# Kernel optimization log

Hardware: AMD Instinct MI355X
Metric: run time of the kernel (lower is better)

Reference implementation:

```python
import jax, jax.numpy as jnp
import numpy as np

D, H, W = 64, 128, 128
NUM_LABELS = 2
NUM_ITERS = 5
SIGMA_SPATIAL_BLUR = 1.0   # sigma for the pure spatial Gaussian filter
BLUR_RADIUS = 2            # 5-tap separable kernel
SIGMA_BILAT_SPATIAL = 1.5  # spatial sigma of bilateral filter
SIGMA_BILAT_RANGE = 0.5    # intensity (range) sigma of bilateral filter
LOG_SQRT_2PI = 0.5 * float(np.log(2.0 * np.pi))


def _shift(x, axis, off):
    # zero-padded shift: out[i] = x[i - off] along `axis` (static off)
    if off == 0:
        return x
    pad = [(0, 0)] * x.ndim
    sl = [slice(None)] * x.ndim
    if off > 0:
        pad[axis] = (off, 0)
        sl[axis] = slice(0, x.shape[axis])
    else:
        pad[axis] = (0, -off)
        sl[axis] = slice(-off, x.shape[axis] - off)
    return jnp.pad(x, pad)[tuple(sl)]


def _shift3(x, dz, dy, dx):
    return _shift(_shift(_shift(x, 2, dz), 3, dy), 4, dx)


_offs = np.arange(-BLUR_RADIUS, BLUR_RADIUS + 1)
_k1d = np.exp(-_offs.astype(np.float64) ** 2 / (2.0 * SIGMA_SPATIAL_BLUR ** 2))
_k1d = (_k1d / _k1d.sum()).astype(np.float32)


def _gaussian_blur3d(x):
    # separable normalized Gaussian over the 3 spatial axes (zero padding)
    for ax in (2, 3, 4):
        x = sum(float(_k1d[i]) * _shift(x, ax, int(_offs[i])) for i in range(len(_offs)))
    return x


def _bilateral_weights(image):
    # precompute 27 neighbor weight maps (image is constant across CRF iterations)
    ws, offsets = [], []
    for dz in (-1, 0, 1):
        for dy in (-1, 0, 1):
            for dx in (-1, 0, 1):
                d2 = float(dz * dz + dy * dy + dx * dx)
                img_s = _shift3(image, dz, dy, dx)
                w = jnp.exp(-d2 / (2.0 * SIGMA_BILAT_SPATIAL ** 2)
                            - (image - img_s) ** 2 / (2.0 * SIGMA_BILAT_RANGE ** 2))
                ws.append(w)
                offsets.append((dz, dy, dx))
    den = sum(ws)  # (1,1,D,H,W), broadcasts over labels
    return ws, den, offsets


def _bilateral_apply(q, ws, den, offsets):
    num = sum(w * _shift3(q, dz, dy, dx) for w, (dz, dy, dx) in zip(ws, offsets))
    return num / den


def _crfrnn(image, logits, unary, spatial_w, bilateral_w, compat):
    ws, den, offsets = _bilateral_weights(image)
    cur = logits
    for _ in range(NUM_ITERS):
        qs = jax.nn.softmax(cur, axis=1)                      # (1,L,D,H,W)
        sp = _gaussian_blur3d(qs)                             # spatial message
        bl = _bilateral_apply(qs, ws, den, offsets)           # bilateral message
        msg = (jnp.einsum('lm,bmdhw->bldhw', spatial_w, sp)
               + jnp.einsum('lm,bmdhw->bldhw', bilateral_w, bl))
        pairwise = jnp.einsum('lm,bmdhw->bldhw', compat, msg)
        cur = unary - pairwise
    return jax.nn.softmax(cur, axis=1)


def setup_inputs() -> dict:
    key = jax.random.key(0)
    k1, k2, k3, k4, k5, k6 = jax.random.split(key, 6)
    image = jax.random.normal(k1, (1, 1, D, H, W), dtype=jnp.float32)
    q = jax.random.uniform(k2, (1, 1, D, H, W), dtype=jnp.float32)
    h = jnp.concatenate([1.0 - q, q], axis=1)                 # (1,2,D,H,W)
    f_1 = jax.random.normal(k3, (1, 1, D, H, W), dtype=jnp.float32)
    w_0 = jnp.zeros((1,), dtype=jnp.float32)
    spatial_ker_weights = jax.random.normal(k4, (NUM_LABELS, NUM_LABELS), dtype=jnp.float32)
    bilateral_ker_weights = jax.random.normal(k5, (NUM_LABELS, NUM_LABELS), dtype=jnp.float32)
    compatibility_matrix = jax.random.normal(k6, (NUM_LABELS, NUM_LABELS), dtype=jnp.float32)
    return {'image': image, 'h': h, 'f_1': f_1, 'w_0': w_0,
            'spatial_ker_weights': spatial_ker_weights,
            'bilateral_ker_weights': bilateral_ker_weights,
            'compatibility_matrix': compatibility_matrix}


def reference(image, h, f_1, w_0, spatial_ker_weights, bilateral_ker_weights, compatibility_matrix):
    logits = h
    log_prob = -0.5 * image * image - LOG_SQRT_2PI           # N(0,1).log_prob(image)
    unary = h * (-(w_0[0] + log_prob - f_1))                 # broadcasts (1,1,..) -> (1,2,..)
    h_new = _crfrnn(image, logits, unary, spatial_ker_weights,
                    bilateral_ker_weights, compatibility_matrix)
    return (h_new, f_1)
```

## Files before the change

kernel.cpp:

```cpp
#include <hip/hip_runtime.h>


#define DD 64
#define HH 128
#define WW 128
#define NN (DD*HH*WW)
#define PAD 264
#define TILE_WU 6912

__device__ __forceinline__ float bfac(int p, int dim) {
    const float K[5] = {0.05448868f, 0.24420134f, 0.40261995f, 0.24420134f, 0.05448868f};
    float s = 0.f;
#pragma unroll
    for (int o = -2; o <= 2; ++o) {
        int pp = p + o;
        s += (pp >= 0 && pp < dim) ? K[o + 2] : 0.f;
    }
    return s;
}

__device__ __forceinline__ void ldrow(const float* p, float* r) {
    float4 a = *(const float4*)p;
    float4 b = *(const float4*)(p + 4);
    r[0] = a.x; r[1] = a.y; r[2] = a.z; r[3] = a.w;
    r[4] = b.x; r[5] = b.y; r[6] = b.z; r[7] = b.w;
}

__global__ __launch_bounds__(256) void crf_pre(
    const float* __restrict__ img, const float* __restrict__ h,
    const float* __restrict__ f1, const float* __restrict__ w0,
    const float* __restrict__ sw, const float* __restrict__ bw,
    const float* __restrict__ cm,
    float* __restrict__ qA, float* __restrict__ P,
    float* __restrict__ M, unsigned int* __restrict__ W)
{
    const float Sc[4] = {1.f, 0.80073740f, 0.64118039f, 0.51341712f};
    __shared__ float ims[10][10][20];

    const int tid = threadIdx.x;
    const int x0 = blockIdx.x * 16, y0 = blockIdx.y * 8, z0 = blockIdx.z * 8;
    const int T = ((int)blockIdx.z * 16 + (int)blockIdx.y) * 8 + (int)blockIdx.x;

    float* imf = &ims[0][0][0];
    for (int idx = tid; idx < 2000; idx += 256) {
        int lz2 = idx / 200, r = idx - lz2 * 200, ly2 = r / 20, lx2 = r - ly2 * 20;
        int gz = z0 + lz2 - 1, gy = y0 + ly2 - 1, gx = x0 + lx2 - 1;
        float v = 0.f;
        if ((unsigned)gz < 64u && (unsigned)gy < 128u && (unsigned)gx < 128u)
            v = img[(gz << 14) + (gy << 7) + gx];
        imf[idx] = v;
    }
    __syncthreads();

    const int lx = (tid & 3) * 4;
    const int ly = (tid >> 2) & 7;
    const int lz = tid >> 5;
    const int x = x0 + lx, y = y0 + ly, z = z0 + lz;
    const int g = (z << 14) + (y << 7) + x;

    const float cd0 = cm[2] - cm[0], cd1 = cm[3] - cm[1];
    const float Ksp = cd0 * sw[0] + cd1 * sw[2];
    const float Kbl = cd0 * bw[0] + cd1 * bw[2];
    const float Bc  = cd0 * (bw[1] - bw[0]) + cd1 * (bw[3] - bw[2]);

    float rowC[8];
    ldrow(&ims[lz + 1][ly + 1][lx], rowC);
    const float Ic[4] = {rowC[1], rowC[2], rowC[3], rowC[4]};

    float den[4] = {0.f, 0.f, 0.f, 0.f}, numi[4] = {0.f, 0.f, 0.f, 0.f};
    unsigned int* __restrict__ Wt = W + T * TILE_WU;

    float rI[8];
#pragma unroll
    for (int r9 = 0; r9 < 9; ++r9) {
        const int dz = r9 / 3 - 1, dy = r9 % 3 - 1;
        ldrow(&ims[lz + 1 + dz][ly + 1 + dy][lx], rI);
        const bool zyin = ((unsigned)(z + dz) < 64u) && ((unsigned)(y + dy) < 128u);
#pragma unroll
        for (int c = 0; c < 3; ++c) {
            const int dx = c - 1;
            const float s = Sc[dz * dz + dy * dy + dx * dx];
            unsigned pack = 0;
#pragma unroll
            for (int xi = 0; xi < 4; ++xi) {
                float dd = Ic[xi] - rI[xi + c];
                float w = s * __expf(-2.f * dd * dd);
                den[xi] += w;
                bool inb = zyin && ((unsigned)(x + xi + dx) < 128u);
                numi[xi] += inb ? w : 0.f;
                pack |= ((unsigned)(w * 255.f + 0.5f)) << (8 * xi);
            }
            Wt[(r9 * 3 + c) * 256 + tid] = pack;
        }
    }

    float4 h0v = *(const float4*)&h[g];
    float4 h1v = *(const float4*)&h[NN + g];
    float4 f1v = *(const float4*)&f1[g];
    const float w00 = w0[0];
    const float bz = bfac(z, 64), by = bfac(y, 128);
    float hh0[4] = {h0v.x, h0v.y, h0v.z, h0v.w};
    float hh1[4] = {h1v.x, h1v.y, h1v.z, h1v.w};
    float ff[4]  = {f1v.x, f1v.y, f1v.z, f1v.w};
    float qv[4], Pv[4], Mv[4];
#pragma unroll
    for (int xi = 0; xi < 4; ++xi) {
        float dq = hh1[xi] - hh0[xi];
        float logp = -0.5f * Ic[xi] * Ic[xi] - 0.91893853320467274f;
        float t = -(w00 + logp - ff[xi]);
        float bones = bz * by * bfac(x + xi, 128);
        qv[xi] = 1.f / (1.f + __expf(-dq));
        Pv[xi] = dq * t - Ksp * bones - Kbl * (numi[xi] / den[xi]);
        Mv[xi] = Bc / (den[xi] * 255.f);
    }
    *(float4*)&qA[g] = {qv[0], qv[1], qv[2], qv[3]};
    *(float4*)&P[g]  = {Pv[0], Pv[1], Pv[2], Pv[3]};
    *(float4*)&M[g]  = {Mv[0], Mv[1], Mv[2], Mv[3]};
}

template <bool LAST>
__global__ __launch_bounds__(256) void crf_iter(
    const float* __restrict__ qsrc, float* __restrict__ qdst,
    const float* __restrict__ P, const float* __restrict__ M,
    const unsigned int* __restrict__ W,
    const float* __restrict__ sw, const float* __restrict__ cm,
    const float* __restrict__ f1, float* __restrict__ out)
{
    const float K0 = 0.05448868f, K1 = 0.24420134f, K2 = 0.40261995f;

    __shared__ float qs[12][12][20];
    __shared__ float t1[12][12][16];
    __shared__ float t2[12][8][16];

    const int tid = threadIdx.x;
    const int x0 = blockIdx.x * 16, y0 = blockIdx.y * 8, zB = blockIdx.z * 8;
    const int T = ((int)blockIdx.z * 16 + (int)blockIdx.y) * 8 + (int)blockIdx.x;

    const float cd0 = cm[2] - cm[0], cd1 = cm[3] - cm[1];
    const float Ac = cd0 * (sw[1] - sw[0]) + cd1 * (sw[3] - sw[2]);

    float* qf = &qs[0][0][0];
    for (int idx = tid; idx < 2880; idx += 256) {
        int lz2 = idx / 240, r = idx - lz2 * 240, ly2 = r / 20, lx2 = r - ly2 * 20;
        int gz = zB + lz2 - 2, gy = y0 + ly2 - 2, gx = x0 + lx2 - 2;
        float v = 0.f;
        if ((unsigned)gz < 64u && (unsigned)gy < 128u && (unsigned)gx < 128u)
            v = qsrc[(gz << 14) + (gy << 7) + gx];
        qf[idx] = v;
    }
    __syncthreads();

    for (int idx = tid; idx < 576; idx += 256) {
        int lz2 = idx / 48, r = idx - lz2 * 48, ly2 = r / 4, c4 = (r - ly2 * 4) * 4;
        const float* row = &qs[lz2][ly2][c4];
        float4 a = *(const float4*)row;
        float4 b = *(const float4*)(row + 4);
        float4 o;
        o.x = K0 * (a.x + b.x) + K1 * (a.y + a.w) + K2 * a.z;
        o.y = K0 * (a.y + b.y) + K1 * (a.z + b.x) + K2 * a.w;
        o.z = K0 * (a.z + b.z) + K1 * (a.w + b.y) + K2 * b.x;
        o.w = K0 * (a.w + b.w) + K1 * (b.x + b.z) + K2 * b.y;
        *(float4*)&t1[lz2][ly2][c4] = o;
    }
    __syncthreads();

    for (int idx = tid; idx < 384; idx += 256) {
        int lz2 = idx / 32, r = idx - lz2 * 32, ly2 = r / 4, c4 = (r - ly2 * 4) * 4;
        float4 r0 = *(const float4*)&t1[lz2][ly2][c4];
        float4 r1 = *(const float4*)&t1[lz2][ly2 + 1][c4];
        float4 r2 = *(const float4*)&t1[lz2][ly2 + 2][c4];
        float4 r3 = *(const float4*)&t1[lz2][ly2 + 3][c4];
        float4 r4 = *(const float4*)&t1[lz2][ly2 + 4][c4];
        float4 o;
        o.x = K0 * (r0.x + r4.x) + K1 * (r1.x + r3.x) + K2 * r2.x;
        o.y = K0 * (r0.y + r4.y) + K1 * (r1.y + r3.y) + K2 * r2.y;
        o.z = K0 * (r0.z + r4.z) + K1 * (r1.z + r3.z) + K2 * r2.z;
        o.w = K0 * (r0.w + r4.w) + K1 * (r1.w + r3.w) + K2 * r2.w;
        *(float4*)&t2[lz2][ly2][c4] = o;
    }
    __syncthreads();

    const int lx = (tid & 3) * 4;
    const int ly = (tid >> 2) & 7;
    const int lz = tid >> 5;

    float4 za = *(const float4*)&t2[lz][ly][lx];
    float4 zb = *(const float4*)&t2[lz + 1][ly][lx];
    float4 zc = *(const float4*)&t2[lz + 2][ly][lx];
    float4 zd = *(const float4*)&t2[lz + 3][ly][lx];
    float4 ze = *(const float4*)&t2[lz + 4][ly][lx];
    float sp[4];
    sp[0] = K0 * (za.x + ze.x) + K1 * (zb.x + zd.x) + K2 * zc.x;
    sp[1] = K0 * (za.y + ze.y) + K1 * (zb.y + zd.y) + K2 * zc.y;
    sp[2] = K0 * (za.z + ze.z) + K1 * (zb.z + zd.z) + K2 * zc.z;
    sp[3] = K0 * (za.w + ze.w) + K1 * (zb.w + zd.w) + K2 * zc.w;

    const int g = ((zB + lz) << 14) + ((y0 + ly) << 7) + (x0 + lx);

    const unsigned int* __restrict__ Wt = W + T * TILE_WU;
    float num[4] = {0.f, 0.f, 0.f, 0.f};
    float qrow[8];
#pragma unroll
    for (int r9 = 0; r9 < 9; ++r9) {
        const int dz = r9 / 3 - 1, dy = r9 % 3 - 1;
        ldrow(&qs[lz + 2 + dz][ly + 2 + dy][lx], qrow);
#pragma unroll
        for (int c = 0; c < 3; ++c) {
            unsigned wv = Wt[(r9 * 3 + c) * 256 + tid];
#pragma unroll
            for (int xi = 0; xi < 4; ++xi)
                num[xi] += (float)((wv >> (8 * xi)) & 0xffu) * qrow[xi + 1 + c];
        }
    }

    float4 Pv = *(const float4*)&P[g];
    float4 Mv = *(const float4*)&M[g];
    float pr[4] = {Pv.x, Pv.y, Pv.z, Pv.w};
    float mv[4] = {Mv.x, Mv.y, Mv.z, Mv.w};
    float qn[4];
#pragma unroll
    for (int xi = 0; xi < 4; ++xi) {
        float dn = pr[xi] - Ac * sp[xi] - mv[xi] * num[xi];
        qn[xi] = 1.f / (1.f + __expf(-dn));
    }

    if (!LAST) {
        float4 o = {qn[0], qn[1], qn[2], qn[3]};
        *(float4*)&qdst[g] = o;
    } else {
        float4 o1 = {qn[0], qn[1], qn[2], qn[3]};
        float4 o0 = {1.f - qn[0], 1.f - qn[1], 1.f - qn[2], 1.f - qn[3]};
        *(float4*)&out[g] = o0;
        *(float4*)&out[NN + g] = o1;
        float4 fv = *(const float4*)&f1[g];
        *(float4*)&out[2 * NN + g] = fv;
    }
}

extern "C" void kernel_launch(void* const* d_in, const int* in_sizes, int n_in,
                              void* d_out, int out_size, void* d_ws, size_t ws_size,
                              hipStream_t stream)
{
    const float* img = (const float*)d_in[0];
    const float* h   = (const float*)d_in[1];
    const float* f1  = (const float*)d_in[2];
    const float* w0  = (const float*)d_in[3];
    const float* sw  = (const float*)d_in[4];
    const float* bw  = (const float*)d_in[5];
    const float* cm  = (const float*)d_in[6];
    float* out = (float*)d_out;

    float* qA = (float*)d_ws;
    float* qB = qA + (NN + PAD);
    float* P  = qB + (NN + PAD);
    float* M  = P + (NN + PAD);
    unsigned int* W = (unsigned int*)(M + (NN + PAD));

    dim3 grid(WW / 16, HH / 8, DD / 8);
    crf_pre<<<grid, 256, 0, stream>>>(img, h, f1, w0, sw, bw, cm, qA, P, M, W);

    crf_iter<false><<<grid, 256, 0, stream>>>(qA, qB, P, M, W, sw, cm, nullptr, nullptr);
    crf_iter<false><<<grid, 256, 0, stream>>>(qB, qA, P, M, W, sw, cm, nullptr, nullptr);
    crf_iter<false><<<grid, 256, 0, stream>>>(qA, qB, P, M, W, sw, cm, nullptr, nullptr);
    crf_iter<false><<<grid, 256, 0, stream>>>(qB, qA, P, M, W, sw, cm, nullptr, nullptr);
    crf_iter<true ><<<grid, 256, 0, stream>>>(qA, nullptr, P, M, W, sw, cm, f1, out);
}
```

Baseline: 161.5 us.

## Store q in zero-padded layout for branchless vectorized halo loads and prefetch weights

Measured after the change: 175.0 us. 1.08x slower.

```diff
diff --git a/kernel.cpp b/kernel.cpp
--- a/kernel.cpp
+++ b/kernel.cpp
@@ -7,6 +7,10 @@
 #define NN (DD*HH*WW)
 #define PAD 264
 #define TILE_WU 6912
+#define XP 136
+#define SLICE (132*136)
+#define QTOT (68*SLICE)
+#define QOFF (2*SLICE + 2*XP + 4)
 
 __device__ __forceinline__ float bfac(int p, int dim) {
     const float K[5] = {0.05448868f, 0.24420134f, 0.40261995f, 0.24420134f, 0.05448868f};
@@ -26,13 +30,14 @@
     r[4] = b.x; r[5] = b.y; r[6] = b.z; r[7] = b.w;
 }
 
-__global__ __launch_bounds__(256) void crf_pre(
+__global__ __launch_bounds__(256, 4) void crf_pre(
     const float* __restrict__ img, const float* __restrict__ h,
     const float* __restrict__ f1, const float* __restrict__ w0,
     const float* __restrict__ sw, const float* __restrict__ bw,
     const float* __restrict__ cm,
-    float* __restrict__ qA, float* __restrict__ P,
-    float* __restrict__ M, unsigned int* __restrict__ W)
+    float* __restrict__ qA, float* __restrict__ qB,
+    float* __restrict__ P, float* __restrict__ M,
+    unsigned int* __restrict__ W, float* __restrict__ out)
 {
     const float Sc[4] = {1.f, 0.80073740f, 0.64118039f, 0.51341712f};
     __shared__ float ims[10][10][20];
@@ -40,6 +45,17 @@
     const int tid = threadIdx.x;
     const int x0 = blockIdx.x * 16, y0 = blockIdx.y * 8, z0 = blockIdx.z * 8;
     const int T = ((int)blockIdx.z * 16 + (int)blockIdx.y) * 8 + (int)blockIdx.x;
+
+    {
+        int gtid = T * 256 + tid;
+        for (int lin = gtid; lin < QTOT; lin += 262144) {
+            int zq = lin / SLICE, r = lin - zq * SLICE;
+            int yq = r / XP, xq = r - yq * XP;
+            bool inter = (zq >= 2 && zq < 66 && yq >= 2 && yq < 130 &&
+                          xq >= 4 && xq < 132);
+            if (!inter) { qA[lin] = 0.f; qB[lin] = 0.f; }
+        }
+    }
 
     float* imf = &ims[0][0][0];
     for (int idx = tid; idx < 2000; idx += 256) {
@@ -52,9 +68,7 @@
     }
     __syncthreads();
 
-    const int lx = (tid & 3) * 4;
-    const int ly = (tid >> 2) & 7;
-    const int lz = tid >> 5;
+    const int lx = (tid & 3) * 4, ly = (tid >> 2) & 7, lz = tid >> 5;
     const int x = x0 + lx, y = y0 + ly, z = z0 + lz;
     const int g = (z << 14) + (y << 7) + x;
 
@@ -66,10 +80,8 @@
     float rowC[8];
     ldrow(&ims[lz + 1][ly + 1][lx], rowC);
     const float Ic[4] = {rowC[1], rowC[2], rowC[3], rowC[4]};
-
     float den[4] = {0.f, 0.f, 0.f, 0.f}, numi[4] = {0.f, 0.f, 0.f, 0.f};
     unsigned int* __restrict__ Wt = W + T * TILE_WU;
-
     float rI[8];
 #pragma unroll
     for (int r9 = 0; r9 < 9; ++r9) {
@@ -97,11 +109,11 @@
     float4 h0v = *(const float4*)&h[g];
     float4 h1v = *(const float4*)&h[NN + g];
     float4 f1v = *(const float4*)&f1[g];
-    const float w00 = w0[0];
-    const float bz = bfac(z, 64), by = bfac(y, 128);
     float hh0[4] = {h0v.x, h0v.y, h0v.z, h0v.w};
     float hh1[4] = {h1v.x, h1v.y, h1v.z, h1v.w};
     float ff[4]  = {f1v.x, f1v.y, f1v.z, f1v.w};
+    const float w00 = w0[0];
+    const float bz = bfac(z, 64), by = bfac(y, 128);
     float qv[4], Pv[4], Mv[4];
 #pragma unroll
     for (int xi = 0; xi < 4; ++xi) {
@@ -113,53 +125,68 @@
         Pv[xi] = dq * t - Ksp * bones - Kbl * (numi[xi] / den[xi]);
         Mv[xi] = Bc / (den[xi] * 255.f);
     }
-    *(float4*)&qA[g] = {qv[0], qv[1], qv[2], qv[3]};
-    *(float4*)&P[g]  = {Pv[0], Pv[1], Pv[2], Pv[3]};
-    *(float4*)&M[g]  = {Mv[0], Mv[1], Mv[2], Mv[3]};
+    *(float4*)&qA[z * SLICE + y * XP + x + QOFF] = {qv[0], qv[1], qv[2], qv[3]};
+    *(float4*)&P[g] = {Pv[0], Pv[1], Pv[2], Pv[3]};
+    *(float4*)&M[g] = {Mv[0], Mv[1], Mv[2], Mv[3]};
+    *(float4*)&out[2 * NN + g] = f1v;
 }
 
 template <bool LAST>
-__global__ __launch_bounds__(256) void crf_iter(
+__global__ __launch_bounds__(256, 4) void crf_iter(
     const float* __restrict__ qsrc, float* __restrict__ qdst,
     const float* __restrict__ P, const float* __restrict__ M,
     const unsigned int* __restrict__ W,
     const float* __restrict__ sw, const float* __restrict__ cm,
-    const float* __restrict__ f1, float* __restrict__ out)
+    float* __restrict__ out)
 {
     const float K0 = 0.05448868f, K1 = 0.24420134f, K2 = 0.40261995f;
 
-    __shared__ float qs[12][12][20];
+    __shared__ float qs[12][12][24];
     __shared__ float t1[12][12][16];
     __shared__ float t2[12][8][16];
 
     const int tid = threadIdx.x;
     const int x0 = blockIdx.x * 16, y0 = blockIdx.y * 8, zB = blockIdx.z * 8;
     const int T = ((int)blockIdx.z * 16 + (int)blockIdx.y) * 8 + (int)blockIdx.x;
+    const int lx = (tid & 3) * 4, ly = (tid >> 2) & 7, lz = tid >> 5;
+    const int g = ((zB + lz) << 14) + ((y0 + ly) << 7) + (x0 + lx);
 
     const float cd0 = cm[2] - cm[0], cd1 = cm[3] - cm[1];
     const float Ac = cd0 * (sw[1] - sw[0]) + cd1 * (sw[3] - sw[2]);
 
-    float* qf = &qs[0][0][0];
-    for (int idx = tid; idx < 2880; idx += 256) {
-        int lz2 = idx / 240, r = idx - lz2 * 240, ly2 = r / 20, lx2 = r - ly2 * 20;
-        int gz = zB + lz2 - 2, gy = y0 + ly2 - 2, gx = x0 + lx2 - 2;
-        float v = 0.f;
-        if ((unsigned)gz < 64u && (unsigned)gy < 128u && (unsigned)gx < 128u)
-            v = qsrc[(gz << 14) + (gy << 7) + gx];
-        qf[idx] = v;
+    const unsigned int* __restrict__ Wt = W + T * TILE_WU;
+    unsigned w27[27];
+#pragma unroll
+    for (int o = 0; o < 27; ++o) w27[o] = Wt[o * 256 + tid];
+    float4 Pv = *(const float4*)&P[g];
+    float4 Mv = *(const float4*)&M[g];
+
+    {
+        const int zb = (zB - 2) * SLICE + (y0 - 2) * XP + (x0 - 4) + QOFF;
+#pragma unroll
+        for (int pass = 0; pass < 4; ++pass) {
+            int i = pass * 256 + tid;
+            if (i < 864) {
+                int lz2 = i / 72, r = i - lz2 * 72;
+                int ly2 = r / 6, lxf = r - ly2 * 6;
+                float4 v = *(const float4*)&qsrc[zb + lz2 * SLICE + ly2 * XP + lxf * 4];
+                *(float4*)&qs[lz2][ly2][lxf * 4] = v;
+            }
+        }
     }
     __syncthreads();
 
     for (int idx = tid; idx < 576; idx += 256) {
         int lz2 = idx / 48, r = idx - lz2 * 48, ly2 = r / 4, c4 = (r - ly2 * 4) * 4;
-        const float* row = &qs[lz2][ly2][c4];
-        float4 a = *(const float4*)row;
-        float4 b = *(const float4*)(row + 4);
+        const float* rp = &qs[lz2][ly2][0];
+        float4 A = *(const float4*)&rp[c4];
+        float4 B = *(const float4*)&rp[c4 + 4];
+        float4 C = *(const float4*)&rp[c4 + 8];
         float4 o;
-        o.x = K0 * (a.x + b.x) + K1 * (a.y + a.w) + K2 * a.z;
-        o.y = K0 * (a.y + b.y) + K1 * (a.z + b.x) + K2 * a.w;
-        o.z = K0 * (a.z + b.z) + K1 * (a.w + b.y) + K2 * b.x;
-        o.w = K0 * (a.w + b.w) + K1 * (b.x + b.z) + K2 * b.y;
+        o.x = K0 * (A.z + B.z) + K1 * (A.w + B.y) + K2 * B.x;
+        o.y = K0 * (A.w + B.w) + K1 * (B.x + B.z) + K2 * B.y;
+        o.z = K0 * (B.x + C.x) + K1 * (B.y + B.w) + K2 * B.z;
+        o.w = K0 * (B.y + C.y) + K1 * (B.z + C.x) + K2 * B.w;
         *(float4*)&t1[lz2][ly2][c4] = o;
     }
     __syncthreads();
@@ -180,60 +207,55 @@
     }
     __syncthreads();
 
-    const int lx = (tid & 3) * 4;
-    const int ly = (tid >> 2) & 7;
-    const int lz = tid >> 5;
-
     float4 za = *(const float4*)&t2[lz][ly][lx];
-    float4 zb = *(const float4*)&t2[lz + 1][ly][lx];
+    float4 zb4 = *(const float4*)&t2[lz + 1][ly][lx];
     float4 zc = *(const float4*)&t2[lz + 2][ly][lx];
     float4 zd = *(const float4*)&t2[lz + 3][ly][lx];
     float4 ze = *(const float4*)&t2[lz + 4][ly][lx];
     float sp[4];
-    sp[0] = K0 * (za.x + ze.x) + K1 * (zb.x + zd.x) + K2 * zc.x;
-    sp[1] = K0 * (za.y + ze.y) + K1 * (zb.y + zd.y) + K2 * zc.y;
-    sp[2] = K0 * (za.z + ze.z) + K1 * (zb.z + zd.z) + K2 * zc.z;
-    sp[3] = K0 * (za.w + ze.w) + K1 * (zb.w + zd.w) + K2 * zc.w;
-
-    const int g = ((zB + lz) << 14) + ((y0 + ly) << 7) + (x0 + lx);
-
-    const unsigned int* __restrict__ Wt = W + T * TILE_WU;
+    sp[0] = K0 * (za.x + ze.x) + K1 * (zb4.x + zd.x) + K2 * zc.x;
+    sp[1] = K0 * (za.y + ze.y) + K1 * (zb4.y + zd.y) + K2 * zc.y;
+    sp[2] = K0 * (za.z + ze.z) + K1 * (zb4.z + zd.z) + K2 * zc.z;
+    sp[3] = K0 * (za.w + ze.w) + K1 * (zb4.w + zd.w) + K2 * zc.w;
+
     float num[4] = {0.f, 0.f, 0.f, 0.f};
-    float qrow[8];
+    float qrow[12];
 #pragma unroll
     for (int r9 = 0; r9 < 9; ++r9) {
         const int dz = r9 / 3 - 1, dy = r9 % 3 - 1;
-        ldrow(&qs[lz + 2 + dz][ly + 2 + dy][lx], qrow);
+        const float* rp2 = &qs[lz + 2 + dz][ly + 2 + dy][0];
+        float4 A = *(const float4*)&rp2[lx];
+        float4 B = *(const float4*)&rp2[lx + 4];
+        float4 C = *(const float4*)&rp2[lx + 8];
+        qrow[0] = A.x; qrow[1] = A.y; qrow[2] = A.z; qrow[3] = A.w;
+        qrow[4] = B.x; qrow[5] = B.y; qrow[6] = B.z; qrow[7] = B.w;
+        qrow[8] = C.x; qrow[9] = C.y; qrow[10] = C.z; qrow[11] = C.w;
 #pragma unroll
         for (int c = 0; c < 3; ++c) {
-            unsigned wv = Wt[(r9 * 3 + c) * 256 + tid];
+            unsigned wv = w27[r9 * 3 + c];
 #pragma unroll
             for (int xi = 0; xi < 4; ++xi)
-                num[xi] += (float)((wv >> (8 * xi)) & 0xffu) * qrow[xi + 1 + c];
-        }
-    }
-
-    float4 Pv = *(const float4*)&P[g];
-    float4 Mv = *(const float4*)&M[g];
-    float pr[4] = {Pv.x, Pv.y, Pv.z, Pv.w};
-    float mv[4] = {Mv.x, Mv.y, Mv.z, Mv.w};
+                num[xi] += (float)((wv >> (8 * xi)) & 0xffu) * qrow[3 + xi + c];
+        }
+    }
+
+    float pr4[4] = {Pv.x, Pv.y, Pv.z, Pv.w};
+    float mv4[4] = {Mv.x, Mv.y, Mv.z, Mv.w};
     float qn[4];
 #pragma unroll
     for (int xi = 0; xi < 4; ++xi) {
-        float dn = pr[xi] - Ac * sp[xi] - mv[xi] * num[xi];
+        float dn = pr4[xi] - Ac * sp[xi] - mv4[xi] * num[xi];
         qn[xi] = 1.f / (1.f + __expf(-dn));
     }
 
     if (!LAST) {
-        float4 o = {qn[0], qn[1], qn[2], qn[3]};
-        *(float4*)&qdst[g] = o;
+        const int ql = (zB + lz) * SLICE + (y0 + ly) * XP + (x0 + lx) + QOFF;
+        *(float4*)&qdst[ql] = {qn[0], qn[1], qn[2], qn[3]};
     } else {
         float4 o1 = {qn[0], qn[1], qn[2], qn[3]};
         float4 o0 = {1.f - qn[0], 1.f - qn[1], 1.f - qn[2], 1.f - qn[3]};
         *(float4*)&out[g] = o0;
         *(float4*)&out[NN + g] = o1;
-        float4 fv = *(const float4*)&f1[g];
-        *(float4*)&out[2 * NN + g] = fv;
     }
 }
 
@@ -251,17 +273,16 @@
     float* out = (float*)d_out;
 
     float* qA = (float*)d_ws;
-    float* qB = qA + (NN + PAD);
-    float* P  = qB + (NN + PAD);
+    float* qB = qA + (QTOT + PAD);
+    float* P  = qB + (QTOT + PAD);
     float* M  = P + (NN + PAD);
     unsigned int* W = (unsigned int*)(M + (NN + PAD));
 
     dim3 grid(WW / 16, HH / 8, DD / 8);
-    crf_pre<<<grid, 256, 0, stream>>>(img, h, f1, w0, sw, bw, cm, qA, P, M, W);
-
-    crf_iter<false><<<grid, 256, 0, stream>>>(qA, qB, P, M, W, sw, cm, nullptr, nullptr);
-    crf_iter<false><<<grid, 256, 0, stream>>>(qB, qA, P, M, W, sw, cm, nullptr, nullptr);
-    crf_iter<false><<<grid, 256, 0, stream>>>(qA, qB, P, M, W, sw, cm, nullptr, nullptr);
-    crf_iter<false><<<grid, 256, 0, stream>>>(qB, qA, P, M, W, sw, cm, nullptr, nullptr);
-    crf_iter<true ><<<grid, 256, 0, stream>>>(qA, nullptr, P, M, W, sw, cm, f1, out);
-}
+    crf_pre<<<grid, 256, 0, stream>>>(img, h, f1, w0, sw, bw, cm, qA, qB, P, M, W, out);
+    crf_iter<false><<<grid, 256, 0, stream>>>(qA, qB, P, M, W, sw, cm, nullptr);
+    crf_iter<false><<<grid, 256, 0, stream>>>(qB, qA, P, M, W, sw, cm, nullptr);
+    crf_iter<false><<<grid, 256, 0, stream>>>(qA, qB, P, M, W, sw, cm, nullptr);
+    crf_iter<false><<<grid, 256, 0, stream>>>(qB, qA, P, M, W, sw, cm, nullptr);
+    crf_iter<true ><<<grid, 256, 0, stream>>>(qA, nullptr, P, M, W, sw, cm, out);
+}
```

## Fuse precompute with first CRF iteration and prefetch weights into registers

Applied to the files above, without the earlier changes.

Measured after the change: 176.8 us. 1.09x slower.

```diff
diff --git a/kernel.cpp b/kernel.cpp
--- a/kernel.cpp
+++ b/kernel.cpp
@@ -26,127 +26,112 @@
     r[4] = b.x; r[5] = b.y; r[6] = b.z; r[7] = b.w;
 }
 
-__global__ __launch_bounds__(256) void crf_pre(
+__global__ __launch_bounds__(256) void crf_pre_it1(
     const float* __restrict__ img, const float* __restrict__ h,
     const float* __restrict__ f1, const float* __restrict__ w0,
     const float* __restrict__ sw, const float* __restrict__ bw,
     const float* __restrict__ cm,
-    float* __restrict__ qA, float* __restrict__ P,
-    float* __restrict__ M, unsigned int* __restrict__ W)
+    float* __restrict__ q1out, float* __restrict__ P,
+    float* __restrict__ M, unsigned int* __restrict__ W,
+    float* __restrict__ out)
 {
+    const float K0 = 0.05448868f, K1 = 0.24420134f, K2 = 0.40261995f;
     const float Sc[4] = {1.f, 0.80073740f, 0.64118039f, 0.51341712f};
-    __shared__ float ims[10][10][20];
+
+    __shared__ float qs[12][12][20];
+    __shared__ float t1[12][12][20];
+    __shared__ float t2[12][8][20];
 
     const int tid = threadIdx.x;
     const int x0 = blockIdx.x * 16, y0 = blockIdx.y * 8, z0 = blockIdx.z * 8;
     const int T = ((int)blockIdx.z * 16 + (int)blockIdx.y) * 8 + (int)blockIdx.x;
-
-    float* imf = &ims[0][0][0];
+    const int lx = (tid & 3) * 4, ly = (tid >> 2) & 7, lz = tid >> 5;
+    const int x = x0 + lx, y = y0 + ly, z = z0 + lz;
+    const int g = (z << 14) + (y << 7) + x;
+
+    const float cd0 = cm[2] - cm[0], cd1 = cm[3] - cm[1];
+    const float Ksp = cd0 * sw[0] + cd1 * sw[2];
+    const float Kbl = cd0 * bw[0] + cd1 * bw[2];
+    const float Bc  = cd0 * (bw[1] - bw[0]) + cd1 * (bw[3] - bw[2]);
+    const float Ac  = cd0 * (sw[1] - sw[0]) + cd1 * (sw[3] - sw[2]);
+
+    float* imsf = &t1[0][0][0];
     for (int idx = tid; idx < 2000; idx += 256) {
         int lz2 = idx / 200, r = idx - lz2 * 200, ly2 = r / 20, lx2 = r - ly2 * 20;
         int gz = z0 + lz2 - 1, gy = y0 + ly2 - 1, gx = x0 + lx2 - 1;
         float v = 0.f;
         if ((unsigned)gz < 64u && (unsigned)gy < 128u && (unsigned)gx < 128u)
             v = img[(gz << 14) + (gy << 7) + gx];
-        imf[idx] = v;
-    }
-    __syncthreads();
-
-    const int lx = (tid & 3) * 4;
-    const int ly = (tid >> 2) & 7;
-    const int lz = tid >> 5;
-    const int x = x0 + lx, y = y0 + ly, z = z0 + lz;
-    const int g = (z << 14) + (y << 7) + x;
-
-    const float cd0 = cm[2] - cm[0], cd1 = cm[3] - cm[1];
-    const float Ksp = cd0 * sw[0] + cd1 * sw[2];
-    const float Kbl = cd0 * bw[0] + cd1 * bw[2];
-    const float Bc  = cd0 * (bw[1] - bw[0]) + cd1 * (bw[3] - bw[2]);
-
-    float rowC[8];
-    ldrow(&ims[lz + 1][ly + 1][lx], rowC);
-    const float Ic[4] = {rowC[1], rowC[2], rowC[3], rowC[4]};
-
-    float den[4] = {0.f, 0.f, 0.f, 0.f}, numi[4] = {0.f, 0.f, 0.f, 0.f};
-    unsigned int* __restrict__ Wt = W + T * TILE_WU;
-
-    float rI[8];
-#pragma unroll
-    for (int r9 = 0; r9 < 9; ++r9) {
-        const int dz = r9 / 3 - 1, dy = r9 % 3 - 1;
-        ldrow(&ims[lz + 1 + dz][ly + 1 + dy][lx], rI);
-        const bool zyin = ((unsigned)(z + dz) < 64u) && ((unsigned)(y + dy) < 128u);
-#pragma unroll
-        for (int c = 0; c < 3; ++c) {
-            const int dx = c - 1;
-            const float s = Sc[dz * dz + dy * dy + dx * dx];
-            unsigned pack = 0;
-#pragma unroll
-            for (int xi = 0; xi < 4; ++xi) {
-                float dd = Ic[xi] - rI[xi + c];
-                float w = s * __expf(-2.f * dd * dd);
-                den[xi] += w;
-                bool inb = zyin && ((unsigned)(x + xi + dx) < 128u);
-                numi[xi] += inb ? w : 0.f;
-                pack |= ((unsigned)(w * 255.f + 0.5f)) << (8 * xi);
-            }
-            Wt[(r9 * 3 + c) * 256 + tid] = pack;
-        }
-    }
-
-    float4 h0v = *(const float4*)&h[g];
-    float4 h1v = *(const float4*)&h[NN + g];
-    float4 f1v = *(const float4*)&f1[g];
-    const float w00 = w0[0];
-    const float bz = bfac(z, 64), by = bfac(y, 128);
-    float hh0[4] = {h0v.x, h0v.y, h0v.z, h0v.w};
-    float hh1[4] = {h1v.x, h1v.y, h1v.z, h1v.w};
-    float ff[4]  = {f1v.x, f1v.y, f1v.z, f1v.w};
-    float qv[4], Pv[4], Mv[4];
-#pragma unroll
-    for (int xi = 0; xi < 4; ++xi) {
-        float dq = hh1[xi] - hh0[xi];
-        float logp = -0.5f * Ic[xi] * Ic[xi] - 0.91893853320467274f;
-        float t = -(w00 + logp - ff[xi]);
-        float bones = bz * by * bfac(x + xi, 128);
-        qv[xi] = 1.f / (1.f + __expf(-dq));
-        Pv[xi] = dq * t - Ksp * bones - Kbl * (numi[xi] / den[xi]);
-        Mv[xi] = Bc / (den[xi] * 255.f);
-    }
-    *(float4*)&qA[g] = {qv[0], qv[1], qv[2], qv[3]};
-    *(float4*)&P[g]  = {Pv[0], Pv[1], Pv[2], Pv[3]};
-    *(float4*)&M[g]  = {Mv[0], Mv[1], Mv[2], Mv[3]};
-}
-
-template <bool LAST>
-__global__ __launch_bounds__(256) void crf_iter(
-    const float* __restrict__ qsrc, float* __restrict__ qdst,
-    const float* __restrict__ P, const float* __restrict__ M,
-    const unsigned int* __restrict__ W,
-    const float* __restrict__ sw, const float* __restrict__ cm,
-    const float* __restrict__ f1, float* __restrict__ out)
-{
-    const float K0 = 0.05448868f, K1 = 0.24420134f, K2 = 0.40261995f;
-
-    __shared__ float qs[12][12][20];
-    __shared__ float t1[12][12][16];
-    __shared__ float t2[12][8][16];
-
-    const int tid = threadIdx.x;
-    const int x0 = blockIdx.x * 16, y0 = blockIdx.y * 8, zB = blockIdx.z * 8;
-    const int T = ((int)blockIdx.z * 16 + (int)blockIdx.y) * 8 + (int)blockIdx.x;
-
-    const float cd0 = cm[2] - cm[0], cd1 = cm[3] - cm[1];
-    const float Ac = cd0 * (sw[1] - sw[0]) + cd1 * (sw[3] - sw[2]);
-
+        imsf[idx] = v;
+    }
     float* qf = &qs[0][0][0];
     for (int idx = tid; idx < 2880; idx += 256) {
         int lz2 = idx / 240, r = idx - lz2 * 240, ly2 = r / 20, lx2 = r - ly2 * 20;
-        int gz = zB + lz2 - 2, gy = y0 + ly2 - 2, gx = x0 + lx2 - 2;
+        int gz = z0 + lz2 - 2, gy = y0 + ly2 - 2, gx = x0 + lx2 - 2;
         float v = 0.f;
-        if ((unsigned)gz < 64u && (unsigned)gy < 128u && (unsigned)gx < 128u)
-            v = qsrc[(gz << 14) + (gy << 7) + gx];
+        if ((unsigned)gz < 64u && (unsigned)gy < 128u && (unsigned)gx < 128u) {
+            int gi = (gz << 14) + (gy << 7) + gx;
+            float dq = h[NN + gi] - h[gi];
+            v = 1.f / (1.f + __expf(-dq));
+        }
         qf[idx] = v;
+    }
+    __syncthreads();
+
+    unsigned w27[27];
+    float pr[4], mv[4];
+    {
+        float rowC[8];
+        ldrow(imsf + ((lz + 1) * 10 + (ly + 1)) * 20 + lx, rowC);
+        const float Ic[4] = {rowC[1], rowC[2], rowC[3], rowC[4]};
+        float den[4] = {0.f, 0.f, 0.f, 0.f}, numi[4] = {0.f, 0.f, 0.f, 0.f};
+        unsigned int* __restrict__ Wt = W + T * TILE_WU;
+        float rI[8];
+#pragma unroll
+        for (int r9 = 0; r9 < 9; ++r9) {
+            const int dz = r9 / 3 - 1, dy = r9 % 3 - 1;
+            ldrow(imsf + ((lz + 1 + dz) * 10 + (ly + 1 + dy)) * 20 + lx, rI);
+            const bool zyin = ((unsigned)(z + dz) < 64u) && ((unsigned)(y + dy) < 128u);
+#pragma unroll
+            for (int c = 0; c < 3; ++c) {
+                const int dx = c - 1;
+                const float s = Sc[dz * dz + dy * dy + dx * dx];
+                unsigned pack = 0;
+#pragma unroll
+                for (int xi = 0; xi < 4; ++xi) {
+                    float dd = Ic[xi] - rI[xi + c];
+                    float w = s * __expf(-2.f * dd * dd);
+                    den[xi] += w;
+                    bool inb = zyin && ((unsigned)(x + xi + dx) < 128u);
+                    numi[xi] += inb ? w : 0.f;
+                    pack |= ((unsigned)(w * 255.f + 0.5f)) << (8 * xi);
+                }
+                unsigned pk = pack;
+                w27[r9 * 3 + c] = pk;
+                Wt[(r9 * 3 + c) * 256 + tid] = pk;
+            }
+        }
+        float4 h0v = *(const float4*)&h[g];
+        float4 h1v = *(const float4*)&h[NN + g];
+        float4 f1v = *(const float4*)&f1[g];
+        float hh0[4] = {h0v.x, h0v.y, h0v.z, h0v.w};
+        float hh1[4] = {h1v.x, h1v.y, h1v.z, h1v.w};
+        float ff[4]  = {f1v.x, f1v.y, f1v.z, f1v.w};
+        const float w00 = w0[0];
+        const float bz = bfac(z, 64), by = bfac(y, 128);
+        float Pv[4], Mv[4];
+#pragma unroll
+        for (int xi = 0; xi < 4; ++xi) {
+            float dq = hh1[xi] - hh0[xi];
+            float logp = -0.5f * Ic[xi] * Ic[xi] - 0.91893853320467274f;
+            float t = -(w00 + logp - ff[xi]);
+            float bones = bz * by * bfac(x + xi, 128);
+            pr[xi] = Pv[xi] = dq * t - Ksp * bones - Kbl * (numi[xi] / den[xi]);
+            mv[xi] = Mv[xi] = Bc / (den[xi] * 255.f);
+        }
+        *(float4*)&P[g] = {Pv[0], Pv[1], Pv[2], Pv[3]};
+        *(float4*)&M[g] = {Mv[0], Mv[1], Mv[2], Mv[3]};
+        *(float4*)&out[2 * NN + g] = f1v;
     }
     __syncthreads();
 
@@ -180,10 +165,6 @@
     }
     __syncthreads();
 
-    const int lx = (tid & 3) * 4;
-    const int ly = (tid >> 2) & 7;
-    const int lz = tid >> 5;
-
     float4 za = *(const float4*)&t2[lz][ly][lx];
     float4 zb = *(const float4*)&t2[lz + 1][ly][lx];
     float4 zc = *(const float4*)&t2[lz + 2][ly][lx];
@@ -195,9 +176,6 @@
     sp[2] = K0 * (za.z + ze.z) + K1 * (zb.z + zd.z) + K2 * zc.z;
     sp[3] = K0 * (za.w + ze.w) + K1 * (zb.w + zd.w) + K2 * zc.w;
 
-    const int g = ((zB + lz) << 14) + ((y0 + ly) << 7) + (x0 + lx);
-
-    const unsigned int* __restrict__ Wt = W + T * TILE_WU;
     float num[4] = {0.f, 0.f, 0.f, 0.f};
     float qrow[8];
 #pragma unroll
@@ -206,34 +184,135 @@
         ldrow(&qs[lz + 2 + dz][ly + 2 + dy][lx], qrow);
 #pragma unroll
         for (int c = 0; c < 3; ++c) {
-            unsigned wv = Wt[(r9 * 3 + c) * 256 + tid];
+            unsigned wv = w27[r9 * 3 + c];
 #pragma unroll
             for (int xi = 0; xi < 4; ++xi)
                 num[xi] += (float)((wv >> (8 * xi)) & 0xffu) * qrow[xi + 1 + c];
         }
     }
 
-    float4 Pv = *(const float4*)&P[g];
-    float4 Mv = *(const float4*)&M[g];
-    float pr[4] = {Pv.x, Pv.y, Pv.z, Pv.w};
-    float mv[4] = {Mv.x, Mv.y, Mv.z, Mv.w};
     float qn[4];
 #pragma unroll
     for (int xi = 0; xi < 4; ++xi) {
         float dn = pr[xi] - Ac * sp[xi] - mv[xi] * num[xi];
         qn[xi] = 1.f / (1.f + __expf(-dn));
     }
+    *(float4*)&q1out[g] = {qn[0], qn[1], qn[2], qn[3]};
+}
+
+template <bool LAST>
+__global__ __launch_bounds__(256) void crf_iter(
+    const float* __restrict__ qsrc, float* __restrict__ qdst,
+    const float* __restrict__ P, const float* __restrict__ M,
+    const unsigned int* __restrict__ W,
+    const float* __restrict__ sw, const float* __restrict__ cm,
+    float* __restrict__ out)
+{
+    const float K0 = 0.05448868f, K1 = 0.24420134f, K2 = 0.40261995f;
+
+    __shared__ float qs[12][12][20];
+    __shared__ float t1[12][12][20];
+    __shared__ float t2[12][8][20];
+
+    const int tid = threadIdx.x;
+    const int x0 = blockIdx.x * 16, y0 = blockIdx.y * 8, zB = blockIdx.z * 8;
+    const int T = ((int)blockIdx.z * 16 + (int)blockIdx.y) * 8 + (int)blockIdx.x;
+    const int lx = (tid & 3) * 4, ly = (tid >> 2) & 7, lz = tid >> 5;
+    const int g = ((zB + lz) << 14) + ((y0 + ly) << 7) + (x0 + lx);
+
+    const float cd0 = cm[2] - cm[0], cd1 = cm[3] - cm[1];
+    const float Ac = cd0 * (sw[1] - sw[0]) + cd1 * (sw[3] - sw[2]);
+
+    const unsigned int* __restrict__ Wt = W + T * TILE_WU;
+    unsigned w27[27];
+#pragma unroll
+    for (int o = 0; o < 27; ++o) w27[o] = Wt[o * 256 + tid];
+    float4 Pv = *(const float4*)&P[g];
+    float4 Mv = *(const float4*)&M[g];
+
+    float* qf = &qs[0][0][0];
+    for (int idx = tid; idx < 2880; idx += 256) {
+        int lz2 = idx / 240, r = idx - lz2 * 240, ly2 = r / 20, lx2 = r - ly2 * 20;
+        int gz = zB + lz2 - 2, gy = y0 + ly2 - 2, gx = x0 + lx2 - 2;
+        float v = 0.f;
+        if ((unsigned)gz < 64u && (unsigned)gy < 128u && (unsigned)gx < 128u)
+            v = qsrc[(gz << 14) + (gy << 7) + gx];
+        qf[idx] = v;
+    }
+    __syncthreads();
+
+    for (int idx = tid; idx < 576; idx += 256) {
+        int lz2 = idx / 48, r = idx - lz2 * 48, ly2 = r / 4, c4 = (r - ly2 * 4) * 4;
+        const float* row = &qs[lz2][ly2][c4];
+        float4 a = *(const float4*)row;
+        float4 b = *(const float4*)(row + 4);
+        float4 o;
+        o.x = K0 * (a.x + b.x) + K1 * (a.y + a.w) + K2 * a.z;
+        o.y = K0 * (a.y + b.y) + K1 * (a.z + b.x) + K2 * a.w;
+        o.z = K0 * (a.z + b.z) + K1 * (a.w + b.y) + K2 * b.x;
+        o.w = K0 * (a.w + b.w) + K1 * (b.x + b.z) + K2 * b.y;
+        *(float4*)&t1[lz2][ly2][c4] = o;
+    }
+    __syncthreads();
+
+    for (int idx = tid; idx < 384; idx += 256) {
+        int lz2 = idx / 32, r = idx - lz2 * 32, ly2 = r / 4, c4 = (r - ly2 * 4) * 4;
+        float4 r0 = *(const float4*)&t1[lz2][ly2][c4];
+        float4 r1 = *(const float4*)&t1[lz2][ly2 + 1][c4];
+        float4 r2 = *(const float4*)&t1[lz2][ly2 + 2][c4];
+        float4 r3 = *(const float4*)&t1[lz2][ly2 + 3][c4];
+        float4 r4 = *(const float4*)&t1[lz2][ly2 + 4][c4];
+        float4 o;
+        o.x = K0 * (r0.x + r4.x) + K1 * (r1.x + r3.x) + K2 * r2.x;
+        o.y = K0 * (r0.y + r4.y) + K1 * (r1.y + r3.y) + K2 * r2.y;
+        o.z = K0 * (r0.z + r4.z) + K1 * (r1.z + r3.z) + K2 * r2.z;
+        o.w = K0 * (r0.w + r4.w) + K1 * (r1.w + r3.w) + K2 * r2.w;
+        *(float4*)&t2[lz2][ly2][c4] = o;
+    }
+    __syncthreads();
+
+    float4 za = *(const float4*)&t2[lz][ly][lx];
+    float4 zb = *(const float4*)&t2[lz + 1][ly][lx];
+    float4 zc = *(const float4*)&t2[lz + 2][ly][lx];
+    float4 zd = *(const float4*)&t2[lz + 3][ly][lx];
+    float4 ze = *(const float4*)&t2[lz + 4][ly][lx];
+    float sp[4];
+    sp[0] = K0 * (za.x + ze.x) + K1 * (zb.x + zd.x) + K2 * zc.x;
+    sp[1] = K0 * (za.y + ze.y) + K1 * (zb.y + zd.y) + K2 * zc.y;
+    sp[2] = K0 * (za.z + ze.z) + K1 * (zb.z + zd.z) + K2 * zc.z;
+    sp[3] = K0 * (za.w + ze.w) + K1 * (zb.w + zd.w) + K2 * zc.w;
+
+    float num[4] = {0.f, 0.f, 0.f, 0.f};
+    float qrow[8];
+#pragma unroll
+    for (int r9 = 0; r9 < 9; ++r9) {
+        const int dz = r9 / 3 - 1, dy = r9 % 3 - 1;
+        ldrow(&qs[lz + 2 + dz][ly + 2 + dy][lx], qrow);
+#pragma unroll
+        for (int c = 0; c < 3; ++c) {
+            unsigned wv = w27[r9 * 3 + c];
+#pragma unroll
+            for (int xi = 0; xi < 4; ++xi)
+                num[xi] += (float)((wv >> (8 * xi)) & 0xffu) * qrow[xi + 1 + c];
+        }
+    }
+
+    float pr4[4] = {Pv.x, Pv.y, Pv.z, Pv.w};
+    float mv4[4] = {Mv.x, Mv.y, Mv.z, Mv.w};
+    float qn[4];
+#pragma unroll
+    for (int xi = 0; xi < 4; ++xi) {
+        float dn = pr4[xi] - Ac * sp[xi] - mv4[xi] * num[xi];
+        qn[xi] = 1.f / (1.f + __expf(-dn));
+    }
 
     if (!LAST) {
-        float4 o = {qn[0], qn[1], qn[2], qn[3]};
-        *(float4*)&qdst[g] = o;
+        *(float4*)&qdst[g] = {qn[0], qn[1], qn[2], qn[3]};
     } else {
         float4 o1 = {qn[0], qn[1], qn[2], qn[3]};
         float4 o0 = {1.f - qn[0], 1.f - qn[1], 1.f - qn[2], 1.f - qn[3]};
         *(float4*)&out[g] = o0;
         *(float4*)&out[NN + g] = o1;
-        float4 fv = *(const float4*)&f1[g];
-        *(float4*)&out[2 * NN + g] = fv;
     }
 }
 
@@ -257,11 +336,9 @@
     unsigned int* W = (unsigned int*)(M + (NN + PAD));
 
     dim3 grid(WW / 16, HH / 8, DD / 8);
-    crf_pre<<<grid, 256, 0, stream>>>(img, h, f1, w0, sw, bw, cm, qA, P, M, W);
-
-    crf_iter<false><<<grid, 256, 0, stream>>>(qA, qB, P, M, W, sw, cm, nullptr, nullptr);
-    crf_iter<false><<<grid, 256, 0, stream>>>(qB, qA, P, M, W, sw, cm, nullptr, nullptr);
-    crf_iter<false><<<grid, 256, 0, stream>>>(qA, qB, P, M, W, sw, cm, nullptr, nullptr);
-    crf_iter<false><<<grid, 256, 0, stream>>>(qB, qA, P, M, W, sw, cm, nullptr, nullptr);
-    crf_iter<true ><<<grid, 256, 0, stream>>>(qA, nullptr, P, M, W, sw, cm, f1, out);
-}
+    crf_pre_it1<<<grid, 256, 0, stream>>>(img, h, f1, w0, sw, bw, cm, qA, P, M, W, out);
+    crf_iter<false><<<grid, 256, 0, stream>>>(qA, qB, P, M, W, sw, cm, nullptr);
+    crf_iter<false><<<grid, 256, 0, stream>>>(qB, qA, P, M, W, sw, cm, nullptr);
+    crf_iter<false><<<grid, 256, 0, stream>>>(qA, qB, P, M, W, sw, cm, nullptr);
+    crf_iter<true ><<<grid, 256, 0, stream>>>(qB, nullptr, P, M, W, sw, cm, out);
+}
```

## Store q tile in fp16 LDS, fuse y/z blur passes, raise occupancy hint

Applied to the files above, without the earlier changes.

After: 185.6 us. 14.9% more time.

```diff
diff --git a/kernel.cpp b/kernel.cpp
--- a/kernel.cpp
+++ b/kernel.cpp
@@ -7,6 +7,9 @@
 #define NN (DD*HH*WW)
 #define PAD 264
 #define TILE_WU 6912
+
+typedef _Float16 hf;
+typedef _Float16 hf4 __attribute__((ext_vector_type(4)));
 
 __device__ __forceinline__ float bfac(int p, int dim) {
     const float K[5] = {0.05448868f, 0.24420134f, 0.40261995f, 0.24420134f, 0.05448868f};
@@ -52,9 +55,7 @@
     }
     __syncthreads();
 
-    const int lx = (tid & 3) * 4;
-    const int ly = (tid >> 2) & 7;
-    const int lz = tid >> 5;
+    const int lx = (tid & 3) * 4, ly = (tid >> 2) & 7, lz = tid >> 5;
     const int x = x0 + lx, y = y0 + ly, z = z0 + lz;
     const int g = (z << 14) + (y << 7) + x;
 
@@ -119,7 +120,7 @@
 }
 
 template <bool LAST>
-__global__ __launch_bounds__(256) void crf_iter(
+__global__ __launch_bounds__(256, 6) void crf_iter(
     const float* __restrict__ qsrc, float* __restrict__ qdst,
     const float* __restrict__ P, const float* __restrict__ M,
     const unsigned int* __restrict__ W,
@@ -127,106 +128,90 @@
     const float* __restrict__ f1, float* __restrict__ out)
 {
     const float K0 = 0.05448868f, K1 = 0.24420134f, K2 = 0.40261995f;
-
-    __shared__ float qs[12][12][20];
-    __shared__ float t1[12][12][16];
-    __shared__ float t2[12][8][16];
+    const float Kz[5] = {K0, K1, K2, K1, K0};
+
+    __shared__ hf    qsH[12][12][20];
+    __shared__ float t1[12][12][20];
 
     const int tid = threadIdx.x;
     const int x0 = blockIdx.x * 16, y0 = blockIdx.y * 8, zB = blockIdx.z * 8;
     const int T = ((int)blockIdx.z * 16 + (int)blockIdx.y) * 8 + (int)blockIdx.x;
+    const int lx = (tid & 3) * 4, ly = (tid >> 2) & 7, lz = tid >> 5;
+    const int g = ((zB + lz) << 14) + ((y0 + ly) << 7) + (x0 + lx);
 
     const float cd0 = cm[2] - cm[0], cd1 = cm[3] - cm[1];
     const float Ac = cd0 * (sw[1] - sw[0]) + cd1 * (sw[3] - sw[2]);
 
-    float* qf = &qs[0][0][0];
+    hf* qf = &qsH[0][0][0];
     for (int idx = tid; idx < 2880; idx += 256) {
         int lz2 = idx / 240, r = idx - lz2 * 240, ly2 = r / 20, lx2 = r - ly2 * 20;
         int gz = zB + lz2 - 2, gy = y0 + ly2 - 2, gx = x0 + lx2 - 2;
         float v = 0.f;
         if ((unsigned)gz < 64u && (unsigned)gy < 128u && (unsigned)gx < 128u)
             v = qsrc[(gz << 14) + (gy << 7) + gx];
-        qf[idx] = v;
+        qf[idx] = (hf)v;
     }
     __syncthreads();
 
     for (int idx = tid; idx < 576; idx += 256) {
         int lz2 = idx / 48, r = idx - lz2 * 48, ly2 = r / 4, c4 = (r - ly2 * 4) * 4;
-        const float* row = &qs[lz2][ly2][c4];
-        float4 a = *(const float4*)row;
-        float4 b = *(const float4*)(row + 4);
+        const hf4* row = (const hf4*)&qsH[lz2][ly2][c4];
+        hf4 a = row[0], b = row[1];
+        float a0 = (float)a.x, a1 = (float)a.y, a2 = (float)a.z, a3 = (float)a.w;
+        float b0 = (float)b.x, b1 = (float)b.y, b2 = (float)b.z, b3 = (float)b.w;
         float4 o;
-        o.x = K0 * (a.x + b.x) + K1 * (a.y + a.w) + K2 * a.z;
-        o.y = K0 * (a.y + b.y) + K1 * (a.z + b.x) + K2 * a.w;
-        o.z = K0 * (a.z + b.z) + K1 * (a.w + b.y) + K2 * b.x;
-        o.w = K0 * (a.w + b.w) + K1 * (b.x + b.z) + K2 * b.y;
+        o.x = K0 * (a0 + b0) + K1 * (a1 + a3) + K2 * a2;
+        o.y = K0 * (a1 + b1) + K1 * (a2 + b0) + K2 * a3;
+        o.z = K0 * (a2 + b2) + K1 * (a3 + b1) + K2 * b0;
+        o.w = K0 * (a3 + b3) + K1 * (b0 + b2) + K2 * b1;
         *(float4*)&t1[lz2][ly2][c4] = o;
     }
     __syncthreads();
 
-    for (int idx = tid; idx < 384; idx += 256) {
-        int lz2 = idx / 32, r = idx - lz2 * 32, ly2 = r / 4, c4 = (r - ly2 * 4) * 4;
-        float4 r0 = *(const float4*)&t1[lz2][ly2][c4];
-        float4 r1 = *(const float4*)&t1[lz2][ly2 + 1][c4];
-        float4 r2 = *(const float4*)&t1[lz2][ly2 + 2][c4];
-        float4 r3 = *(const float4*)&t1[lz2][ly2 + 3][c4];
-        float4 r4 = *(const float4*)&t1[lz2][ly2 + 4][c4];
-        float4 o;
-        o.x = K0 * (r0.x + r4.x) + K1 * (r1.x + r3.x) + K2 * r2.x;
-        o.y = K0 * (r0.y + r4.y) + K1 * (r1.y + r3.y) + K2 * r2.y;
-        o.z = K0 * (r0.z + r4.z) + K1 * (r1.z + r3.z) + K2 * r2.z;
-        o.w = K0 * (r0.w + r4.w) + K1 * (r1.w + r3.w) + K2 * r2.w;
-        *(float4*)&t2[lz2][ly2][c4] = o;
-    }
-    __syncthreads();
-
-    const int lx = (tid & 3) * 4;
-    const int ly = (tid >> 2) & 7;
-    const int lz = tid >> 5;
-
-    float4 za = *(const float4*)&t2[lz][ly][lx];
-    float4 zb = *(const float4*)&t2[lz + 1][ly][lx];
-    float4 zc = *(const float4*)&t2[lz + 2][ly][lx];
-    float4 zd = *(const float4*)&t2[lz + 3][ly][lx];
-    float4 ze = *(const float4*)&t2[lz + 4][ly][lx];
-    float sp[4];
-    sp[0] = K0 * (za.x + ze.x) + K1 * (zb.x + zd.x) + K2 * zc.x;
-    sp[1] = K0 * (za.y + ze.y) + K1 * (zb.y + zd.y) + K2 * zc.y;
-    sp[2] = K0 * (za.z + ze.z) + K1 * (zb.z + zd.z) + K2 * zc.z;
-    sp[3] = K0 * (za.w + ze.w) + K1 * (zb.w + zd.w) + K2 * zc.w;
-
-    const int g = ((zB + lz) << 14) + ((y0 + ly) << 7) + (x0 + lx);
+    float sp[4] = {0.f, 0.f, 0.f, 0.f};
+#pragma unroll
+    for (int a = 0; a < 5; ++a) {
+#pragma unroll
+        for (int b = 0; b < 5; ++b) {
+            const float kk = Kz[a] * Kz[b];
+            float4 v = *(const float4*)&t1[lz + a][ly + b][lx];
+            sp[0] += kk * v.x; sp[1] += kk * v.y;
+            sp[2] += kk * v.z; sp[3] += kk * v.w;
+        }
+    }
 
     const unsigned int* __restrict__ Wt = W + T * TILE_WU;
     float num[4] = {0.f, 0.f, 0.f, 0.f};
-    float qrow[8];
 #pragma unroll
     for (int r9 = 0; r9 < 9; ++r9) {
         const int dz = r9 / 3 - 1, dy = r9 % 3 - 1;
-        ldrow(&qs[lz + 2 + dz][ly + 2 + dy][lx], qrow);
+        const hf4* rp = (const hf4*)&qsH[lz + 2 + dz][ly + 2 + dy][lx];
+        hf4 A = rp[0], B = rp[1];
+        float q1 = (float)A.y, q2 = (float)A.z, q3 = (float)A.w;
+        float q4 = (float)B.x, q5 = (float)B.y, q6 = (float)B.z;
+        float qv[6] = {q1, q2, q3, q4, q5, q6};
 #pragma unroll
         for (int c = 0; c < 3; ++c) {
             unsigned wv = Wt[(r9 * 3 + c) * 256 + tid];
 #pragma unroll
             for (int xi = 0; xi < 4; ++xi)
-                num[xi] += (float)((wv >> (8 * xi)) & 0xffu) * qrow[xi + 1 + c];
+                num[xi] += (float)((wv >> (8 * xi)) & 0xffu) * qv[xi + c];
         }
     }
 
     float4 Pv = *(const float4*)&P[g];
     float4 Mv = *(const float4*)&M[g];
-    float pr[4] = {Pv.x, Pv.y, Pv.z, Pv.w};
-    float mv[4] = {Mv.x, Mv.y, Mv.z, Mv.w};
+    float pr4[4] = {Pv.x, Pv.y, Pv.z, Pv.w};
+    float mv4[4] = {Mv.x, Mv.y, Mv.z, Mv.w};
     float qn[4];
 #pragma unroll
     for (int xi = 0; xi < 4; ++xi) {
-        float dn = pr[xi] - Ac * sp[xi] - mv[xi] * num[xi];
+        float dn = pr4[xi] - Ac * sp[xi] - mv4[xi] * num[xi];
         qn[xi] = 1.f / (1.f + __expf(-dn));
     }
 
     if (!LAST) {
-        float4 o = {qn[0], qn[1], qn[2], qn[3]};
-        *(float4*)&qdst[g] = o;
+        *(float4*)&qdst[g] = {qn[0], qn[1], qn[2], qn[3]};
     } else {
         float4 o1 = {qn[0], qn[1], qn[2], qn[3]};
         float4 o0 = {1.f - qn[0], 1.f - qn[1], 1.f - qn[2], 1.f - qn[3]};
```
